# Kernel tuning notes

Hardware: AMD Instinct MI355X
Metric: run time of the kernel (lower is better)

The kernel has to match this reference:

```python
import jax, jax.numpy as jnp
import numpy as np

B, T, D, H = 2, 2048, 1024, 16
HS = D // H  # head_size = 64
EPS = 1e-5


def layernorm(x, g, b):
    mu = jnp.mean(x, axis=-1, keepdims=True)
    var = jnp.var(x, axis=-1, keepdims=True)
    return (x - mu) * jax.lax.rsqrt(var + EPS) * g + b


def setup_inputs() -> dict:
    key = jax.random.key(0)
    ks = jax.random.split(key, 12)
    s = lambda fan: 1.0 / np.sqrt(fan)
    inp = {
        "x": jax.random.normal(ks[0], (B, T, D), dtype=jnp.float32),
        "mask": jnp.ones((T, T), dtype=jnp.int32),
        # per-head Q/K/V weights stacked over heads: [H, D, HS] (bias=False)
        "Wq": jax.random.normal(ks[1], (H, D, HS), dtype=jnp.float32) * s(D),
        "Wk": jax.random.normal(ks[2], (H, D, HS), dtype=jnp.float32) * s(D),
        "Wv": jax.random.normal(ks[3], (H, D, HS), dtype=jnp.float32) * s(D),
        "Wp": jax.random.normal(ks[4], (H * HS, D), dtype=jnp.float32) * s(H * HS),
        "bp": jnp.zeros((D,), dtype=jnp.float32),
        "W1": jax.random.normal(ks[5], (D, 4 * D), dtype=jnp.float32) * s(D),
        "b1": jnp.zeros((4 * D,), dtype=jnp.float32),
        "W2": jax.random.normal(ks[6], (4 * D, D), dtype=jnp.float32) * s(4 * D),
        "b2": jnp.zeros((D,), dtype=jnp.float32),
        "g1": jnp.ones((D,), dtype=jnp.float32),
        "be1": jnp.zeros((D,), dtype=jnp.float32),
        "g2": jnp.ones((D,), dtype=jnp.float32),
        "be2": jnp.zeros((D,), dtype=jnp.float32),
    }
    return inp


def reference(x, mask, Wq, Wk, Wv, Wp, bp, W1, b1, W2, b2, g1, be1, g2, be2):
    # --- self-attention sublayer (pre-LN), dropout=0 (eval) ---
    h = layernorm(x, g1, be1)                         # [B,T,D]; memory == x here
    q = jnp.einsum('btd,hds->bhts', h, Wq)            # [B,H,T,HS]
    k = jnp.einsum('btd,hds->bhts', h, Wk)
    v = jnp.einsum('btd,hds->bhts', h, Wv)
    scale = 1.0 / np.sqrt(HS)
    wei = jnp.einsum('bhts,bhus->bhtu', q, k) * scale  # [B,H,T,T]
    wei = jnp.where(mask == 0, -jnp.inf, wei)          # mask [T,T] broadcasts
    wei = jax.nn.softmax(wei, axis=-1)
    attn = jnp.einsum('bhtu,bhus->bhts', wei, v)       # [B,H,T,HS]
    attn = attn.transpose(0, 2, 1, 3).reshape(B, T, H * HS)  # concat heads
    x = x + attn @ Wp + bp
    # --- feed-forward sublayer (pre-LN) ---
    h2 = layernorm(x, g2, be2)
    x = x + jax.nn.relu(h2 @ W1 + b1) @ W2 + b2
    return x
```

## Files before the change

### kernel.cpp

```cpp
#include <hip/hip_runtime.h>
#include <hip/hip_bf16.h>


#define T_SEQ 2048
#define DMODEL 1024
#define NHEAD 16

typedef __attribute__((ext_vector_type(8))) short short8;
typedef __attribute__((ext_vector_type(4))) float f32x4;

__device__ __forceinline__ short f2bf(float f) {
  unsigned u = __builtin_bit_cast(unsigned, f);
  u += 0x7fff + ((u >> 16) & 1);
  return (short)(u >> 16);
}

__device__ __forceinline__ float fexp2(float x) {
#if __has_builtin(__builtin_amdgcn_exp2f)
  return __builtin_amdgcn_exp2f(x);
#else
  return exp2f(x);
#endif
}

__global__ __launch_bounds__(256)
void transpose_f32_bf16(const float* __restrict__ src, short* __restrict__ dst, int R, int C) {
  __shared__ float tile[32][33];
  size_t zoff = (size_t)blockIdx.z * R * C;
  src += zoff; dst += zoff;
  int c0 = blockIdx.x * 32, r0 = blockIdx.y * 32;
  int tx = threadIdx.x, ty = threadIdx.y;
  #pragma unroll
  for (int i = 0; i < 32; i += 8)
    tile[ty + i][tx] = src[(size_t)(r0 + ty + i) * C + c0 + tx];
  __syncthreads();
  #pragma unroll
  for (int i = 0; i < 32; i += 8)
    dst[(size_t)(c0 + ty + i) * R + r0 + tx] = f2bf(tile[tx][ty + i]);
}

__global__ __launch_bounds__(256)
void ln_kernel(const float* __restrict__ x, const float* __restrict__ g,
               const float* __restrict__ b, short* __restrict__ out) {
  int row = blockIdx.x;
  int tid = threadIdx.x;
  const float4 v = ((const float4*)(x + (size_t)row * DMODEL))[tid];
  float s  = v.x + v.y + v.z + v.w;
  float s2 = v.x * v.x + v.y * v.y + v.z * v.z + v.w * v.w;
  #pragma unroll
  for (int off = 1; off < 64; off <<= 1) {
    s  += __shfl_xor(s, off);
    s2 += __shfl_xor(s2, off);
  }
  __shared__ float red[8];
  int wid = tid >> 6, lane = tid & 63;
  if (lane == 0) { red[wid] = s; red[4 + wid] = s2; }
  __syncthreads();
  s  = red[0] + red[1] + red[2] + red[3];
  s2 = red[4] + red[5] + red[6] + red[7];
  float mu = s * (1.f / DMODEL);
  float var = s2 * (1.f / DMODEL) - mu * mu;
  float rstd = rsqrtf(var + 1e-5f);
  const float4 gg = ((const float4*)g)[tid];
  const float4 bb = ((const float4*)b)[tid];
  short4 o;
  o.x = f2bf((v.x - mu) * rstd * gg.x + bb.x);
  o.y = f2bf((v.y - mu) * rstd * gg.y + bb.y);
  o.z = f2bf((v.z - mu) * rstd * gg.z + bb.z);
  o.w = f2bf((v.w - mu) * rstd * gg.w + bb.w);
  *(short4*)(out + (size_t)row * DMODEL + tid * 4) = o;
}

template<int EPI, int BN, int PIPE>
__global__ __launch_bounds__(256)
void gemm_bt(const short* __restrict__ A, const short* __restrict__ Bt,
             int M, int N, int K,
             const float* __restrict__ bias, const float* __restrict__ resid,
             float* __restrict__ outF, short* __restrict__ outB,
             short* __restrict__ outQ, short* __restrict__ outK, short* __restrict__ outV) {
  constexpr int NBUF = PIPE ? 2 : 1;
  constexpr int NFR = BN / 32;
  __shared__ short ldsA[NBUF][128 * 64];
  __shared__ short ldsB[NBUF][BN * 64];
  int tid = threadIdx.x, lane = tid & 63, wid = tid >> 6;

  int bid = blockIdx.y * gridDim.x + blockIdx.x;
  int nwg = gridDim.x * gridDim.y;
  int swz = (bid & 7) * (nwg >> 3) + (bid >> 3);
  int m0 = (swz / gridDim.x) * 128, n0 = (swz % gridDim.x) * BN;

  int wr = wid >> 1, wc = wid & 1;
  f32x4 acc[4][NFR];
  #pragma unroll
  for (int i = 0; i < 4; i++)
    #pragma unroll
    for (int j = 0; j < NFR; j++)
      #pragma unroll
      for (int e = 0; e < 4; e++) acc[i][j][e] = 0.f;

  int lrow = lane >> 3;
  int schunk = (lane & 7) ^ lrow;

  auto stage = [&](int buf, int k0) {
    #pragma unroll
    for (int it = 0; it < 4; it++) {
      int rA = (wid * 4 + it) * 8;
      const short* gA = A + (size_t)(m0 + rA + lrow) * K + k0 + schunk * 8;
      __builtin_amdgcn_global_load_lds((const __attribute__((address_space(1))) void*)gA,
          (__attribute__((address_space(3))) void*)(&ldsA[buf][rA * 64]), 16, 0, 0);
    }
    #pragma unroll
    for (int it = 0; it < NFR; it++) {
      int rB = (wid * NFR + it) * 8;
      const short* gB = Bt + (size_t)(n0 + rB + lrow) * K + k0 + schunk * 8;
      __builtin_amdgcn_global_load_lds((const __attribute__((address_space(1))) void*)gB,
          (__attribute__((address_space(3))) void*)(&ldsB[buf][rB * 64]), 16, 0, 0);
    }
  };

  auto compute = [&](int buf) {
    #pragma unroll
    for (int kk = 0; kk < 2; kk++) {
      short8 af[4], bf[NFR];
      #pragma unroll
      for (int m = 0; m < 4; m++) {
        int row = wr * 64 + m * 16 + (lane & 15);
        int c = kk * 4 + (lane >> 4);
        af[m] = *(const short8*)((const char*)&ldsA[buf][0] + row * 128 + ((c ^ (row & 7)) << 4));
      }
      #pragma unroll
      for (int n = 0; n < NFR; n++) {
        int row = wc * (BN / 2) + n * 16 + (lane & 15);
        int c = kk * 4 + (lane >> 4);
        bf[n] = *(const short8*)((const char*)&ldsB[buf][0] + row * 128 + ((c ^ (row & 7)) << 4));
      }
      #pragma unroll
      for (int m = 0; m < 4; m++)
        #pragma unroll
        for (int n = 0; n < NFR; n++)
          acc[m][n] = __builtin_amdgcn_mfma_f32_16x16x32_bf16(af[m], bf[n], acc[m][n], 0, 0, 0);
    }
  };

  if constexpr (PIPE) {
    int NT = K >> 6, cur = 0;
    stage(0, 0);
    for (int t = 0; t < NT; t++) {
      __syncthreads();
      if (t + 1 < NT) stage(cur ^ 1, (t + 1) * 64);
      compute(cur);
      cur ^= 1;
    }
  } else {
    for (int k0 = 0; k0 < K; k0 += 64) {
      __syncthreads();
      stage(0, k0);
      __syncthreads();
      compute(0);
    }
  }

  #pragma unroll
  for (int m = 0; m < 4; m++) {
    #pragma unroll
    for (int n = 0; n < NFR; n++) {
      #pragma unroll
      for (int j = 0; j < 4; j++) {
        int row = m0 + wr * 64 + m * 16 + (lane >> 4) * 4 + j;
        int col = n0 + wc * (BN / 2) + n * 16 + (lane & 15);
        float v = acc[m][n][j];
        if constexpr (EPI == 0) {
          int which = col >> 10, r = col & 1023, h = r >> 6, s = r & 63;
          int bb = row >> 11, tt = row & 2047;
          if (which == 2)
            outV[((size_t)(bb * NHEAD + h) * 64 + s) * T_SEQ + tt] = f2bf(v);
          else {
            size_t idx = ((size_t)(bb * NHEAD + h) * T_SEQ + tt) * 64 + s;
            (which == 0 ? outQ : outK)[idx] = f2bf(v);
          }
        } else if constexpr (EPI == 1) {
          size_t idx = (size_t)row * N + col;
          outF[idx] = v + bias[col] + resid[idx];
        } else if constexpr (EPI == 2) {
          float t = v + bias[col];
          outB[(size_t)row * N + col] = f2bf(t > 0.f ? t : 0.f);
        } else {
          size_t idx = (size_t)row * N + col;
          outF[idx] = v + bias[col] + outF[idx];
        }
      }
    }
  }
}

__global__ __launch_bounds__(256)
void attn_kernel(const short* __restrict__ Qg, const short* __restrict__ Kg,
                 const short* __restrict__ Vt, short* __restrict__ Og) {
  __shared__ short kbuf[2][64 * 64];
  __shared__ short vbuf[2][64 * 64];
  __shared__ short pbuf[4][16 * 64];
  int qtile = blockIdx.x, bh = blockIdx.y;
  int tid = threadIdx.x, lane = tid & 63, wid = tid >> 6;
  const short* Qh = Qg + (size_t)bh * T_SEQ * 64;
  const short* Kh = Kg + (size_t)bh * T_SEQ * 64;
  const short* Vh = Vt + (size_t)bh * 64 * T_SEQ;
  int qbase = qtile * 64 + wid * 16;
  int g = lane >> 4, q15 = lane & 15;
  int lrow8 = lane >> 3, schunk = (lane & 7) ^ lrow8;

  short8 qf[2];
  #pragma unroll
  for (int kk = 0; kk < 2; kk++)
    qf[kk] = *(const short8*)(Qh + (size_t)(qbase + q15) * 64 + kk * 32 + g * 8);

  f32x4 o[4];
  #pragma unroll
  for (int n = 0; n < 4; n++)
    #pragma unroll
    for (int j = 0; j < 4; j++) o[n][j] = 0.f;
  float m2 = -1e30f, l = 0.f;
  const float C = 0.18033688f;

#define ATTN_STAGE(buf, kt2) do {                                                          \
    const short* gk = Kh + (size_t)((kt2) * 64 + 16 * wid + lrow8) * 64 + schunk * 8;      \
    __builtin_amdgcn_global_load_lds((const __attribute__((address_space(1))) void*)gk,    \
        (__attribute__((address_space(3))) void*)(&kbuf[buf][(16 * wid) * 64]), 16, 0, 0); \
    __builtin_amdgcn_global_load_lds((const __attribute__((address_space(1))) void*)(gk + 8 * 64), \
        (__attribute__((address_space(3))) void*)(&kbuf[buf][(16 * wid + 8) * 64]), 16, 0, 0);     \
    const short* gv = Vh + (size_t)(16 * wid + lrow8) * T_SEQ + (kt2) * 64 + schunk * 8;   \
    __builtin_amdgcn_global_load_lds((const __attribute__((address_space(1))) void*)gv,    \
        (__attribute__((address_space(3))) void*)(&vbuf[buf][(16 * wid) * 64]), 16, 0, 0); \
    __builtin_amdgcn_global_load_lds((const __attribute__((address_space(1))) void*)(gv + 8 * T_SEQ), \
        (__attribute__((address_space(3))) void*)(&vbuf[buf][(16 * wid + 8) * 64]), 16, 0, 0);        \
  } while (0)

  ATTN_STAGE(0, 0);
  __syncthreads();

  for (int kt = 0; kt < T_SEQ / 64; kt++) {
    int cur = kt & 1;
    if (kt < T_SEQ / 64 - 1) ATTN_STAGE(cur ^ 1, kt + 1);

    f32x4 sacc[4];
    #pragma unroll
    for (int n = 0; n < 4; n++)
      #pragma unroll
      for (int j = 0; j < 4; j++) sacc[n][j] = 0.f;
    #pragma unroll
    for (int n = 0; n < 4; n++) {
      int row = n * 16 + q15;
      #pragma unroll
      for (int kk = 0; kk < 2; kk++) {
        short8 kf = *(const short8*)((const char*)kbuf[cur] + row * 128 + (((kk * 4 + g) ^ (q15 & 7)) << 4));
        sacc[n] = __builtin_amdgcn_mfma_f32_16x16x32_bf16(kf, qf[kk], sacc[n], 0, 0, 0);
      }
    }

    float tm = -1e30f;
    #pragma unroll
    for (int n = 0; n < 4; n++)
      #pragma unroll
      for (int j = 0; j < 4; j++) tm = fmaxf(tm, sacc[n][j]);
    tm = fmaxf(tm, __shfl_xor(tm, 16));
    tm = fmaxf(tm, __shfl_xor(tm, 32));
    float mnew = fmaxf(m2, tm * C);
    float rs = 0.f;
    #pragma unroll
    for (int n = 0; n < 4; n++) {
      float p0 = fexp2(fmaf(sacc[n][0], C, -mnew));
      float p1 = fexp2(fmaf(sacc[n][1], C, -mnew));
      float p2 = fexp2(fmaf(sacc[n][2], C, -mnew));
      float p3 = fexp2(fmaf(sacc[n][3], C, -mnew));
      rs += (p0 + p1) + (p2 + p3);
      short4 pw;
      pw.x = f2bf(p0); pw.y = f2bf(p1); pw.z = f2bf(p2); pw.w = f2bf(p3);
      int pchunk = 2 * n + (g >> 1);
      int poff = q15 * 128 + ((pchunk ^ (q15 & 7)) << 4) + ((g & 1) << 3);
      *(short4*)((char*)pbuf[wid] + poff) = pw;
    }
    rs += __shfl_xor(rs, 16);
    rs += __shfl_xor(rs, 32);
    float alpha = fexp2(m2 - mnew);
    m2 = mnew;
    l = l * alpha + rs;
    float ab[4];
    #pragma unroll
    for (int j = 0; j < 4; j++) ab[j] = __shfl(alpha, g * 4 + j);
    #pragma unroll
    for (int n = 0; n < 4; n++)
      #pragma unroll
      for (int j = 0; j < 4; j++) o[n][j] *= ab[j];

    short8 pf[2];
    #pragma unroll
    for (int kk = 0; kk < 2; kk++)
      pf[kk] = *(const short8*)((char*)pbuf[wid] + q15 * 128 + ((((kk * 4 + g)) ^ (q15 & 7)) << 4));
    #pragma unroll
    for (int n = 0; n < 4; n++) {
      int row = n * 16 + q15;
      #pragma unroll
      for (int kk = 0; kk < 2; kk++) {
        short8 vf = *(const short8*)((const char*)vbuf[cur] + row * 128 + (((kk * 4 + g) ^ (q15 & 7)) << 4));
        o[n] = __builtin_amdgcn_mfma_f32_16x16x32_bf16(pf[kk], vf, o[n], 0, 0, 0);
      }
    }
    __syncthreads();
  }
#undef ATTN_STAGE

  float rinv = 1.f / l;
  float rb[4];
  #pragma unroll
  for (int j = 0; j < 4; j++) rb[j] = __shfl(rinv, g * 4 + j);
  int b = bh >> 4, h = bh & 15;
  #pragma unroll
  for (int j = 0; j < 4; j++) {
    #pragma unroll
    for (int n = 0; n < 4; n++) {
      int q = qbase + g * 4 + j;
      int col = h * 64 + n * 16 + q15;
      Og[(size_t)(b * T_SEQ + q) * DMODEL + col] = f2bf(o[n][j] * rb[j]);
    }
  }
}

extern "C" void kernel_launch(void* const* d_in, const int* in_sizes, int n_in,
                              void* d_out, int out_size, void* d_ws, size_t ws_size,
                              hipStream_t stream) {
  const float* x   = (const float*)d_in[0];
  const float* Wq  = (const float*)d_in[2];
  const float* Wk  = (const float*)d_in[3];
  const float* Wv  = (const float*)d_in[4];
  const float* Wp  = (const float*)d_in[5];
  const float* bp  = (const float*)d_in[6];
  const float* W1  = (const float*)d_in[7];
  const float* b1  = (const float*)d_in[8];
  const float* W2  = (const float*)d_in[9];
  const float* b2  = (const float*)d_in[10];
  const float* g1  = (const float*)d_in[11];
  const float* be1 = (const float*)d_in[12];
  const float* g2  = (const float*)d_in[13];
  const float* be2 = (const float*)d_in[14];
  float* out = (float*)d_out;

  char* ws = (char*)d_ws;
  const size_t MB = 1u << 20;
  short* h1    = (short*)(ws + 0);
  short* WqkvT = (short*)(ws + 8 * MB);
  short* Qg    = (short*)(ws + 14 * MB);
  short* Kg    = (short*)(ws + 22 * MB);
  short* Vt    = (short*)(ws + 30 * MB);
  short* attnO = (short*)(ws + 38 * MB);
  short* WpT   = (short*)(ws + 46 * MB);
  short* W1T   = (short*)(ws + 8 * MB);
  short* a1    = (short*)(ws + 16 * MB);
  short* W2T   = (short*)(ws + 48 * MB);

  dim3 blkT(32, 8);
  transpose_f32_bf16<<<dim3(2, 32, 16), blkT, 0, stream>>>(Wq, WqkvT, 1024, 64);
  transpose_f32_bf16<<<dim3(2, 32, 16), blkT, 0, stream>>>(Wk, WqkvT + 1024 * 1024, 1024, 64);
  transpose_f32_bf16<<<dim3(2, 32, 16), blkT, 0, stream>>>(Wv, WqkvT + 2 * 1024 * 1024, 1024, 64);
  transpose_f32_bf16<<<dim3(32, 32, 1), blkT, 0, stream>>>(Wp, WpT, 1024, 1024);

  ln_kernel<<<4096, 256, 0, stream>>>(x, g1, be1, h1);
  gemm_bt<0, 128, 0><<<dim3(24, 32), 256, 0, stream>>>(h1, WqkvT, 4096, 3072, 1024,
      nullptr, nullptr, nullptr, nullptr, Qg, Kg, Vt);
  attn_kernel<<<dim3(32, 32), 256, 0, stream>>>(Qg, Kg, Vt, attnO);
  gemm_bt<1, 64, 1><<<dim3(16, 32), 256, 0, stream>>>(attnO, WpT, 4096, 1024, 1024,
      bp, x, out, nullptr, nullptr, nullptr, nullptr);

  transpose_f32_bf16<<<dim3(128, 32, 1), blkT, 0, stream>>>(W1, W1T, 1024, 4096);
  ln_kernel<<<4096, 256, 0, stream>>>(out, g2, be2, h1);
  gemm_bt<2, 128, 0><<<dim3(32, 32), 256, 0, stream>>>(h1, W1T, 4096, 4096, 1024,
      b1, nullptr, nullptr, a1, nullptr, nullptr, nullptr);
  transpose_f32_bf16<<<dim3(32, 128, 1), blkT, 0, stream>>>(W2, W2T, 4096, 1024);
  gemm_bt<3, 64, 1><<<dim3(16, 32), 256, 0, stream>>>(a1, W2T, 4096, 1024, 4096,
      b2, nullptr, out, nullptr, nullptr, nullptr, nullptr);
}
```

Before: 402.5 us.

## Use lazy softmax rescaling and packed bf16 conversion in attention

Replaces the per-tile online-softmax max reduction and O rescale with a lazy scheme. The running max is fixed after the first key tile, and rescaling happens only when some probability in the wave exceeds a threshold. The row-sum cross-lane reduction moves to the end of the loop, and the P conversion uses the hardware packed bf16 convert instruction instead of manual rounding. This removes shuffles, max reductions and multiplies from the inner loop, but lets probabilities grow up to 256x before renormalising, which relies on fp32/bf16 headroom.

```diff
diff --git a/kernel.cpp b/kernel.cpp
--- a/kernel.cpp
+++ b/kernel.cpp
@@ -21,6 +21,12 @@
 #else
   return exp2f(x);
 #endif
+}
+
+__device__ __forceinline__ unsigned cvt_pk_bf16(float lo, float hi) {
+  unsigned r;
+  asm("v_cvt_pk_bf16_f32 %0, %1, %2" : "=v"(r) : "v"(lo), "v"(hi));
+  return r;
 }
 
 __global__ __launch_bounds__(256)
@@ -218,7 +224,7 @@
   for (int n = 0; n < 4; n++)
     #pragma unroll
     for (int j = 0; j < 4; j++) o[n][j] = 0.f;
-  float m2 = -1e30f, l = 0.f;
+  float m2 = 0.f, lsum = 0.f;
   const float C = 0.18033688f;
 
 #define ATTN_STAGE(buf, kt2) do {                                                          \
@@ -256,40 +262,59 @@
       }
     }
 
-    float tm = -1e30f;
-    #pragma unroll
-    for (int n = 0; n < 4; n++)
-      #pragma unroll
-      for (int j = 0; j < 4; j++) tm = fmaxf(tm, sacc[n][j]);
-    tm = fmaxf(tm, __shfl_xor(tm, 16));
-    tm = fmaxf(tm, __shfl_xor(tm, 32));
-    float mnew = fmaxf(m2, tm * C);
-    float rs = 0.f;
+    float p[4][4];
+    if (kt == 0) {
+      float tm = -1e30f;
+      #pragma unroll
+      for (int n = 0; n < 4; n++)
+        #pragma unroll
+        for (int j = 0; j < 4; j++) tm = fmaxf(tm, sacc[n][j]);
+      tm = fmaxf(tm, __shfl_xor(tm, 16));
+      tm = fmaxf(tm, __shfl_xor(tm, 32));
+      m2 = tm * C;
+      #pragma unroll
+      for (int n = 0; n < 4; n++)
+        #pragma unroll
+        for (int j = 0; j < 4; j++) p[n][j] = fexp2(fmaf(sacc[n][j], C, -m2));
+    } else {
+      float pmax = 0.f;
+      #pragma unroll
+      for (int n = 0; n < 4; n++)
+        #pragma unroll
+        for (int j = 0; j < 4; j++) {
+          p[n][j] = fexp2(fmaf(sacc[n][j], C, -m2));
+          pmax = fmaxf(pmax, p[n][j]);
+        }
+      if (!__all(pmax <= 256.f)) {
+        float pm = fmaxf(pmax, __shfl_xor(pmax, 16));
+        pm = fmaxf(pm, __shfl_xor(pm, 32));
+        float delta = fmaxf(__log2f(pm), 0.f);
+        float alpha = fexp2(-delta);
+        m2 += delta;
+        lsum *= alpha;
+        #pragma unroll
+        for (int n = 0; n < 4; n++)
+          #pragma unroll
+          for (int j = 0; j < 4; j++) p[n][j] *= alpha;
+        float ab[4];
+        #pragma unroll
+        for (int j = 0; j < 4; j++) ab[j] = __shfl(alpha, g * 4 + j);
+        #pragma unroll
+        for (int n = 0; n < 4; n++)
+          #pragma unroll
+          for (int j = 0; j < 4; j++) o[n][j] *= ab[j];
+      }
+    }
     #pragma unroll
     for (int n = 0; n < 4; n++) {
-      float p0 = fexp2(fmaf(sacc[n][0], C, -mnew));
-      float p1 = fexp2(fmaf(sacc[n][1], C, -mnew));
-      float p2 = fexp2(fmaf(sacc[n][2], C, -mnew));
-      float p3 = fexp2(fmaf(sacc[n][3], C, -mnew));
-      rs += (p0 + p1) + (p2 + p3);
-      short4 pw;
-      pw.x = f2bf(p0); pw.y = f2bf(p1); pw.z = f2bf(p2); pw.w = f2bf(p3);
+      lsum += (p[n][0] + p[n][1]) + (p[n][2] + p[n][3]);
+      uint2 pw;
+      pw.x = cvt_pk_bf16(p[n][0], p[n][1]);
+      pw.y = cvt_pk_bf16(p[n][2], p[n][3]);
       int pchunk = 2 * n + (g >> 1);
       int poff = q15 * 128 + ((pchunk ^ (q15 & 7)) << 4) + ((g & 1) << 3);
-      *(short4*)((char*)pbuf[wid] + poff) = pw;
-    }
-    rs += __shfl_xor(rs, 16);
-    rs += __shfl_xor(rs, 32);
-    float alpha = fexp2(m2 - mnew);
-    m2 = mnew;
-    l = l * alpha + rs;
-    float ab[4];
-    #pragma unroll
-    for (int j = 0; j < 4; j++) ab[j] = __shfl(alpha, g * 4 + j);
-    #pragma unroll
-    for (int n = 0; n < 4; n++)
-      #pragma unroll
-      for (int j = 0; j < 4; j++) o[n][j] *= ab[j];
+      *(uint2*)((char*)pbuf[wid] + poff) = pw;
+    }
 
     short8 pf[2];
     #pragma unroll
@@ -308,6 +333,9 @@
   }
 #undef ATTN_STAGE
 
+  float l = lsum;
+  l += __shfl_xor(l, 16);
+  l += __shfl_xor(l, 32);
   float rinv = 1.f / l;
   float rb[4];
   #pragma unroll
```

Result: faster. 380.3 us (-5.5%).
